# Optimization experiments

Hardware: AMD Instinct MI355X
Metric: run time of the kernel (lower is better)

## Reference

```python
import jax, jax.numpy as jnp
import numpy as np

N, E, G = 50000, 800000, 64          # nodes, edges, graphs in batch
F, HG, HL = 64, 128, 128             # node feat, graph hidden, lin hidden
AVG_LOG = float(np.log(9.0))         # from deg histogram [0]*8+[1]: log(8+1)


def setup_inputs() -> dict:
    key = jax.random.key(0)
    ks = jax.random.split(key, 24)
    def w(k, shape):
        return 0.1 * jax.random.normal(k, shape, jnp.float32)
    return {
        "x": jax.random.normal(ks[0], (N, F), jnp.float32),
        "edge_index": jax.random.randint(ks[1], (2, E), 0, N),
        "edge_attr": jax.random.normal(ks[2], (E, 1), jnp.float32),
        "batch": jnp.sort(jax.random.randint(ks[3], (N,), 0, G)),
        # PNAConv params (towers=1, pre_layers=1, post_layers=1, edge_dim=1)
        "W_edge": w(ks[4], (1, F)),      "b_edge": w(ks[5], (F,)),
        "W_pre": w(ks[6], (3 * F, F)),   "b_pre": w(ks[7], (F,)),
        "W_post": w(ks[8], (13 * F, HG)), "b_post": w(ks[9], (HG,)),
        "W_lin": w(ks[10], (HG, HG)),    "b_lin": w(ks[11], (HG,)),
        # bn1 / fc2 / bn2
        "g1": jnp.ones((HG,)), "be1": jnp.zeros((HG,)),
        "W2": w(ks[12], (HG, HL)), "b2": w(ks[13], (HL,)),
        "g2": jnp.ones((HL,)), "be2": jnp.zeros((HL,)),
        # one resnet block: fc/bn/fc/bn
        "Wr1": w(ks[14], (HL, HL)), "br1": w(ks[15], (HL,)),
        "gr1": jnp.ones((HL,)), "ber1": jnp.zeros((HL,)),
        "Wr2": w(ks[16], (HL, HL)), "br2": w(ks[17], (HL,)),
        "gr2": jnp.ones((HL,)), "ber2": jnp.zeros((HL,)),
        "W_out": w(ks[18], (HL, 1)), "b_out": w(ks[19], (1,)),
    }


def _bn(z, g, b):
    # BatchNorm1d, training mode: biased batch stats, eps=1e-5
    mu = z.mean(0)
    var = ((z - mu) ** 2).mean(0)
    return (z - mu) * jax.lax.rsqrt(var + 1e-5) * g + b


def _pna(x, edge_index, edge_attr, W_edge, b_edge, W_pre, b_pre,
         W_post, b_post, W_lin, b_lin):
    src, dst = edge_index[0], edge_index[1]  # messages flow j->i, aggregate at dst
    e = edge_attr @ W_edge + b_edge                               # [E, F]
    m = jnp.concatenate([x[dst], x[src], e], -1) @ W_pre + b_pre  # [E, F]
    ones_e = jnp.ones((m.shape[0],), m.dtype)
    cnt = jax.ops.segment_sum(ones_e, dst, N)                     # in-degree
    cnt1 = jnp.maximum(cnt, 1.0)
    mean = jax.ops.segment_sum(m, dst, N) / cnt1[:, None]
    mean2 = jax.ops.segment_sum(m * m, dst, N) / cnt1[:, None]
    std = jnp.sqrt(jax.nn.relu(mean2 - mean * mean) + 1e-5)
    has = (cnt > 0)[:, None]
    mn = jnp.where(has, jax.ops.segment_min(m, dst, N), 0.0)
    mx = jnp.where(has, jax.ops.segment_max(m, dst, N), 0.0)
    agg = jnp.concatenate([mean, mn, mx, std], -1)                # [N, 4F]
    amp = (jnp.log(cnt1 + 1.0) / AVG_LOG)[:, None]                # amplification scaler
    out = jnp.concatenate([agg, agg * amp, agg / amp], -1)        # [N, 12F]
    out = jnp.concatenate([x, out], -1) @ W_post + b_post         # [N, HG]
    return out @ W_lin + b_lin                                    # [N, HG]


def reference(x, edge_index, edge_attr, batch,
              W_edge, b_edge, W_pre, b_pre, W_post, b_post, W_lin, b_lin,
              g1, be1, W2, b2, g2, be2,
              Wr1, br1, gr1, ber1, Wr2, br2, gr2, ber2,
              W_out, b_out):
    h = _pna(x, edge_index, edge_attr, W_edge, b_edge, W_pre, b_pre,
             W_post, b_post, W_lin, b_lin)
    # global_mean_pool over graphs
    gc = jnp.maximum(jax.ops.segment_sum(jnp.ones((h.shape[0],), h.dtype), batch, G), 1.0)
    z = jax.ops.segment_sum(h, batch, G) / gc[:, None]            # [G, HG]
    z = jax.nn.relu(_bn(z, g1, be1))
    z = jax.nn.relu(_bn(z @ W2 + b2, g2, be2))
    r = z
    z = jax.nn.relu(_bn(z @ Wr1 + br1, gr1, ber1))
    z = jax.nn.relu(_bn(z @ Wr2 + br2, gr2, ber2) + r)
    return z @ W_out + b_out                                      # [G, 1]
```

## Files before the change

### kernel.cpp

```cpp
#include <hip/hip_runtime.h>
#include <hip/hip_bf16.h>

using bf16 = __hip_bfloat16;

#define F 64
#define HG 128
#define HL 128
#define AVG_LOG_INV 0.45511961331341866f
#define BSH 5
#define BNODES 32
#define BCAP 1024
#define BTILE 8192
#define NBMAX 1664

typedef short short8 __attribute__((ext_vector_type(8)));
typedef float floatx4 __attribute__((ext_vector_type(4)));

__device__ __forceinline__ float b2f(bf16 v) { return __bfloat162float(v); }
__device__ __forceinline__ bf16 f2b(float v) { return __float2bfloat16(v); }
__device__ __forceinline__ short f2bs(float v) { bf16 h = f2b(v); return *(short*)&h; }

__device__ __forceinline__ unsigned packbf2(float x, float y) {
    bf16 a = f2b(x), b = f2b(y);
    unsigned short ua = *(unsigned short*)&a, ub = *(unsigned short*)&b;
    return ((unsigned)ub << 16) | (unsigned)ua;
}

__device__ __forceinline__ float wave_sum(float v) {
    #pragma unroll
    for (int m = 32; m > 0; m >>= 1) v += __shfl_xor(v, m);
    return v;
}

__global__ void k_ab_mfma(const float* __restrict__ x, const float* __restrict__ W_pre,
                          bf16* __restrict__ AB, int N,
                          int* __restrict__ gcur, float* __restrict__ gfeat,
                          int* __restrict__ gcnt, int NB, int GF, int G,
                          const float* __restrict__ W_edge, const float* __restrict__ b_edge,
                          const float* __restrict__ b_pre, float* __restrict__ uc) {
    int gtid = blockIdx.x * blockDim.x + threadIdx.x;
    int gstr = gridDim.x * blockDim.x;
    for (int i = gtid; i < GF; i += gstr) gfeat[i] = 0.f;
    for (int i = gtid; i < NB; i += gstr) gcur[i] = 0;
    for (int i = gtid; i < G; i += gstr) gcnt[i] = 0;
    if (blockIdx.x == 0 && threadIdx.x < 64) {
        int f = threadIdx.x;
        float u = 0.f, c = b_pre[f];
        for (int k = 0; k < 64; k++) {
            float w3 = W_pre[(128 + k) * 64 + f];
            u += W_edge[k] * w3;
            c += b_edge[k] * w3;
        }
        uc[f] = u; uc[64 + f] = c;
    }

    __shared__ unsigned short wt[128 * 72];
    for (int idx = threadIdx.x; idx < 8192; idx += 256) {
        int k = idx >> 7, m = idx & 127;
        float v = W_pre[((m & 64) + k) * 64 + (m & 63)];
        wt[m * 72 + k] = (unsigned short)f2bs(v);
    }
    __syncthreads();

    int lane = threadIdx.x & 63;
    int row = lane & 15, quad = lane >> 4;
    int w = (blockIdx.x * blockDim.x + threadIdx.x) >> 6;
    int nwaves = (gridDim.x * blockDim.x) >> 6;
    int ntiles = (N + 15) >> 4;

    for (int tile = w; tile < ntiles; tile += nwaves) {
        int m0 = tile << 4;
        int node_a = m0 + row; if (node_a >= N) node_a = N - 1;
        short8 a[2];
        #pragma unroll
        for (int h = 0; h < 2; h++) {
            const float* xp = x + (size_t)node_a * 64 + h * 32 + quad * 8;
            floatx4 v0 = *(const floatx4*)xp;
            floatx4 v1 = *(const floatx4*)(xp + 4);
            #pragma unroll
            for (int j = 0; j < 4; j++) { a[h][j] = f2bs(v0[j]); a[h][4 + j] = f2bs(v1[j]); }
        }
        #pragma unroll
        for (int t = 0; t < 8; t++) {
            int fbase = t * 16;
            floatx4 c = {0.f, 0.f, 0.f, 0.f};
            #pragma unroll
            for (int h = 0; h < 2; h++) {
                short8 b = *(const short8*)(wt + (fbase + row) * 72 + h * 32 + quad * 8);
                c = __builtin_amdgcn_mfma_f32_16x16x32_bf16(a[h], b, c, 0, 0, 0);
            }
            #pragma unroll
            for (int r = 0; r < 4; r++) {
                int node = m0 + quad * 4 + r;
                if (node < N) AB[(size_t)node * 128 + fbase + row] = f2b(c[r]);
            }
        }
    }
}

__global__ void k_bucket(const int* __restrict__ ei, const float* __restrict__ ea,
                         int* __restrict__ gcur, int2* __restrict__ gout,
                         int E, int NB) {
    __shared__ int2 recs[BTILE];
    __shared__ int hist[NBMAX], gst[NBMAX], lrk[NBMAX];
    int t = threadIdx.x;
    for (int b = t; b < NB; b += 1024) hist[b] = 0;
    __syncthreads();
    int base = blockIdx.x * BTILE;
    int lim = E - base; if (lim > BTILE) lim = BTILE;
    int nq = lim >> 2;
    const int4* src4 = (const int4*)(ei + base);
    const int4* dst4 = (const int4*)(ei + E + base);
    const float4* ea4 = (const float4*)(ea + base);
    for (int q = t; q < nq; q += 1024) {
        int4 s = src4[q], d = dst4[q];
        float4 v = ea4[q];
        int i = q * 4;
        recs[i]     = make_int2((d.x << 16) | s.x, __float_as_int(v.x));
        recs[i + 1] = make_int2((d.y << 16) | s.y, __float_as_int(v.y));
        recs[i + 2] = make_int2((d.z << 16) | s.z, __float_as_int(v.z));
        recs[i + 3] = make_int2((d.w << 16) | s.w, __float_as_int(v.w));
        atomicAdd(&hist[d.x >> BSH], 1);
        atomicAdd(&hist[d.y >> BSH], 1);
        atomicAdd(&hist[d.z >> BSH], 1);
        atomicAdd(&hist[d.w >> BSH], 1);
    }
    for (int i = (nq << 2) + t; i < lim; i += 1024) {
        int e = base + i;
        int src = ei[e], dst = ei[E + e];
        recs[i] = make_int2((dst << 16) | src, __float_as_int(ea[e]));
        atomicAdd(&hist[dst >> BSH], 1);
    }
    __syncthreads();
    for (int b = t; b < NB; b += 1024) {
        int h = hist[b];
        lrk[b] = 0;
        gst[b] = (h > 0) ? atomicAdd(&gcur[b], h) : 0;
    }
    __syncthreads();
    for (int i = t; i < lim; i += 1024) {
        int2 r = recs[i];
        int b = ((unsigned)r.x) >> (16 + BSH);
        int k = atomicAdd(&lrk[b], 1);
        int pos = gst[b] + k;
        if (pos < BCAP) gout[(size_t)b * BCAP + pos] = r;
    }
}

__global__ void k_edge(const bf16* __restrict__ AB, const int2* __restrict__ gout,
                       const int* __restrict__ gcur, const float* __restrict__ uc,
                       bf16* __restrict__ agg, float* __restrict__ ampv, int N) {
    __shared__ int2 recs[BCAP], sortd[BCAP];
    __shared__ int ncnt[BNODES], nofs[BNODES], nrank[BNODES];
    int t = threadIdx.x;
    int b = blockIdx.x;
    int nn = N - b * BNODES; if (nn > BNODES) nn = BNODES;
    int ecnt = gcur[b]; if (ecnt > BCAP) ecnt = BCAP;

    for (int i = t; i < ecnt; i += 512) recs[i] = gout[(size_t)b * BCAP + i];
    if (t < BNODES) { ncnt[t] = 0; nrank[t] = 0; }
    __syncthreads();
    for (int i = t; i < ecnt; i += 512)
        atomicAdd(&ncnt[((unsigned)recs[i].x >> 16) & (BNODES - 1)], 1);
    __syncthreads();
    if (t < BNODES) {
        int v = ncnt[t], inc = v;
        #pragma unroll
        for (int m = 1; m < BNODES; m <<= 1) { int u = __shfl_up(inc, m); if (t >= m) inc += u; }
        nofs[t] = inc - v;
    }
    __syncthreads();
    for (int i = t; i < ecnt; i += 512) {
        int2 r = recs[i];
        int nl = ((unsigned)r.x >> 16) & (BNODES - 1);
        int k = atomicAdd(&nrank[nl], 1);
        sortd[nofs[nl] + k] = r;
    }
    __syncthreads();

    int lane = t & 63, w = t >> 6;
    int half = lane & 31, hi32 = lane >> 5;
    float2 u2 = *(const float2*)(uc + 2 * half);
    float2 c2 = *(const float2*)(uc + 64 + 2 * half);

    for (int nl = w; nl < nn; nl += 8) {
        int n = b * BNODES + nl;
        int lo = nofs[nl], cnt = ncnt[nl], hi = lo + cnt;

        unsigned apack = *(const unsigned*)(AB + (size_t)n * 128 + 2 * half);
        float acx = __uint_as_float(apack << 16) + c2.x;
        float acy = __uint_as_float(apack & 0xffff0000u) + c2.y;

        float sx = 0.f, sy = 0.f, qx = 0.f, qy = 0.f;
        float mnx = 3.4e38f, mny = 3.4e38f, mxx = -3.4e38f, mxy = -3.4e38f;

        auto acc2 = [&](unsigned bp, float eav) {
            float bx = __uint_as_float(bp << 16);
            float by = __uint_as_float(bp & 0xffff0000u);
            float m0 = fmaf(eav, u2.x, acx) + bx;
            float m1 = fmaf(eav, u2.y, acy) + by;
            sx += m0; qx = fmaf(m0, m0, qx);
            sy += m1; qy = fmaf(m1, m1, qy);
            mnx = fminf(mnx, m0); mxx = fmaxf(mxx, m0);
            mny = fminf(mny, m1); mxy = fmaxf(mxy, m1);
        };
        auto gaddr = [&](int sn) {
            return (const unsigned*)(AB + (size_t)sn * 128 + 64 + 2 * half);
        };

        for (int base = lo; base < hi; base += 64) {
            int nb = hi - base; if (nb > 64) nb = 64;
            int2 rec = (lane < nb) ? sortd[base + lane] : make_int2(0, 0);
            int vsn = rec.x & 0xFFFF;
            float vea = __int_as_float(rec.y);
            int i = 0;
            for (; i + 8 <= nb; i += 8) {
                int sn0 = __shfl(vsn, i + hi32);
                int sn1 = __shfl(vsn, i + 2 + hi32);
                int sn2 = __shfl(vsn, i + 4 + hi32);
                int sn3 = __shfl(vsn, i + 6 + hi32);
                float e0 = __shfl(vea, i + hi32);
                float e1 = __shfl(vea, i + 2 + hi32);
                float e2 = __shfl(vea, i + 4 + hi32);
                float e3 = __shfl(vea, i + 6 + hi32);
                unsigned b0 = *gaddr(sn0);
                unsigned b1 = *gaddr(sn1);
                unsigned b2 = *gaddr(sn2);
                unsigned b3 = *gaddr(sn3);
                acc2(b0, e0); acc2(b1, e1); acc2(b2, e2); acc2(b3, e3);
            }
            for (; i + 2 <= nb; i += 2) {
                int   sn = __shfl(vsn, i + hi32);
                float ev = __shfl(vea, i + hi32);
                acc2(*gaddr(sn), ev);
            }
            if (i < nb) {
                int   sn = __shfl(vsn, i);
                float ev = __shfl(vea, i);
                unsigned bp = *gaddr(sn);
                if (hi32 == 0) acc2(bp, ev);
            }
        }
        sx += __shfl_xor(sx, 32); sy += __shfl_xor(sy, 32);
        qx += __shfl_xor(qx, 32); qy += __shfl_xor(qy, 32);
        mnx = fminf(mnx, __shfl_xor(mnx, 32)); mny = fminf(mny, __shfl_xor(mny, 32));
        mxx = fmaxf(mxx, __shfl_xor(mxx, 32)); mxy = fmaxf(mxy, __shfl_xor(mxy, 32));

        float c1 = (cnt > 0) ? (float)cnt : 1.f;
        float inv = 1.f / c1;
        float mex = sx * inv, mey = sy * inv;
        float vx = qx * inv - mex * mex; if (vx < 0.f) vx = 0.f;
        float vy = qy * inv - mey * mey; if (vy < 0.f) vy = 0.f;
        float sdx = sqrtf(vx + 1e-5f), sdy = sqrtf(vy + 1e-5f);
        if (cnt == 0) { mnx = mny = mxx = mxy = 0.f; }

        size_t ob = (size_t)n * 256 + 2 * half;
        if (hi32 == 0) {
            *(unsigned*)(agg + ob)       = packbf2(mex, mey);
            *(unsigned*)(agg + ob + 64)  = packbf2(mnx, mny);
        } else {
            *(unsigned*)(agg + ob + 128) = packbf2(mxx, mxy);
            *(unsigned*)(agg + ob + 192) = packbf2(sdx, sdy);
        }
        if (lane == 0) ampv[n] = logf(c1 + 1.f) * AVG_LOG_INV;
    }
}

__global__ void k_greduce2(const float* __restrict__ x, const bf16* __restrict__ agg,
                           const float* __restrict__ ampv, const int* __restrict__ batch,
                           float* __restrict__ gfeat, int* __restrict__ gcnt,
                           int N, int chunk) {
    int t = threadIdx.x;
    int lo = blockIdx.x * chunk;
    int hi = lo + chunk; if (hi > N) hi = N;
    if (lo >= hi) return;
    int curg = batch[lo];
    float s1 = 0.f, s2 = 0.f, s3 = 0.f, sx = 0.f;
    int cnt = 0;
    for (int n = lo; n < hi; n++) {
        int g = batch[n];
        if (g != curg) {
            float* gf = gfeat + (size_t)curg * 832;
            unsafeAtomicAdd(&gf[64 + t], s1);
            unsafeAtomicAdd(&gf[320 + t], s2);
            unsafeAtomicAdd(&gf[576 + t], s3);
            if (t < 64) unsafeAtomicAdd(&gf[t], sx);
            if (t == 0) atomicAdd(&gcnt[curg], cnt);
            s1 = s2 = s3 = sx = 0.f; cnt = 0; curg = g;
        }
        float amp = ampv[n];
        float av = b2f(agg[(size_t)n * 256 + t]);
        s1 += av; s2 += av * amp; s3 += av / amp;
        if (t < 64) sx += x[(size_t)n * 64 + t];
        cnt++;
    }
    float* gf = gfeat + (size_t)curg * 832;
    unsafeAtomicAdd(&gf[64 + t], s1);
    unsafeAtomicAdd(&gf[320 + t], s2);
    unsafeAtomicAdd(&gf[576 + t], s3);
    if (t < 64) unsafeAtomicAdd(&gf[t], sx);
    if (t == 0) atomicAdd(&gcnt[curg], cnt);
}

__global__ void k_post1(const float* __restrict__ gfeat, const int* __restrict__ gcnt,
                        const float* __restrict__ W_post, const float* __restrict__ b_post,
                        const float* __restrict__ W_lin, const float* __restrict__ b_lin,
                        float* __restrict__ Zin) {
    int g = blockIdx.x, j = threadIdx.x;
    __shared__ float feat[832];
    __shared__ float z1[128];
    int cg = gcnt[g];
    float r = 1.f / ((cg > 0) ? (float)cg : 1.f);
    for (int i = j; i < 832; i += 128) feat[i] = gfeat[(size_t)g * 832 + i] * r;
    __syncthreads();
    float acc = b_post[j];
    for (int k = 0; k < 832; k++) acc += feat[k] * W_post[k * 128 + j];
    z1[j] = acc;
    __syncthreads();
    float a2 = b_lin[j];
    for (int k = 0; k < 128; k++) a2 += z1[k] * W_lin[k * 128 + j];
    if (cg == 0) a2 = 0.f;
    Zin[g * 128 + j] = a2;
}

__global__ void k_mlpcol(const float* __restrict__ in, const float* __restrict__ W,
                         const float* __restrict__ bias,
                         const float* __restrict__ gamma, const float* __restrict__ beta,
                         const float* __restrict__ res,
                         const float* __restrict__ g_in, const float* __restrict__ be_in,
                         float* __restrict__ outp) {
    __shared__ float A[64 * 129];
    __shared__ float part[4 * 64];
    int t = threadIdx.x;
    int j = blockIdx.x;

    for (int i = t; i < 8192; i += 256) A[(i >> 7) * 129 + (i & 127)] = in[i];
    __syncthreads();

    if (g_in) {
        if (t < 128) {
            int c = t;
            float mu = 0.f;
            for (int r = 0; r < 64; r++) mu += A[r * 129 + c];
            mu *= (1.f / 64.f);
            float var = 0.f;
            for (int r = 0; r < 64; r++) { float d = A[r * 129 + c] - mu; var += d * d; }
            var *= (1.f / 64.f);
            float sc = rsqrtf(var + 1e-5f) * g_in[c], sh = be_in[c];
            for (int r = 0; r < 64; r++) {
                float v = (A[r * 129 + c] - mu) * sc + sh;
                A[r * 129 + c] = v > 0.f ? v : 0.f;
            }
        }
        __syncthreads();
    }

    int r = t & 63, q = t >> 6;
    float acc = 0.f;
    int k0 = q * 32;
    #pragma unroll
    for (int k = 0; k < 32; k++) acc += A[r * 129 + k0 + k] * W[(k0 + k) * 128 + j];
    part[q * 64 + r] = acc;
    __syncthreads();

    if (t < 64) {
        float v = part[t] + part[64 + t] + part[128 + t] + part[192 + t] + bias[j];
        float mu = wave_sum(v) * (1.f / 64.f);
        float d = v - mu;
        float var = wave_sum(d * d) * (1.f / 64.f);
        float o = d * rsqrtf(var + 1e-5f) * gamma[j] + beta[j];
        if (res) o += res[t * 128 + j];
        outp[t * 128 + j] = o > 0.f ? o : 0.f;
    }
}

__global__ void k_out(const float* __restrict__ z4, const float* __restrict__ W_out,
                      const float* b_out, float* __restrict__ out) {
    int g = threadIdx.x;
    float acc = b_out[0];
    for (int j = 0; j < 128; j++) acc += z4[g * 128 + j] * W_out[j];
    out[g] = acc;
}

extern "C" void kernel_launch(void* const* d_in, const int* in_sizes, int n_in,
                              void* d_out, int out_size, void* d_ws, size_t ws_size,
                              hipStream_t stream) {
    const float* x      = (const float*)d_in[0];
    const int*   ei     = (const int*)d_in[1];
    const float* ea     = (const float*)d_in[2];
    const int*   batch  = (const int*)d_in[3];
    const float* W_edge = (const float*)d_in[4];
    const float* b_edge = (const float*)d_in[5];
    const float* W_pre  = (const float*)d_in[6];
    const float* b_pre  = (const float*)d_in[7];
    const float* W_post = (const float*)d_in[8];
    const float* b_post = (const float*)d_in[9];
    const float* W_lin  = (const float*)d_in[10];
    const float* b_lin  = (const float*)d_in[11];
    const float* g1     = (const float*)d_in[12];
    const float* be1    = (const float*)d_in[13];
    const float* W2     = (const float*)d_in[14];
    const float* b2     = (const float*)d_in[15];
    const float* g2     = (const float*)d_in[16];
    const float* be2    = (const float*)d_in[17];
    const float* Wr1    = (const float*)d_in[18];
    const float* br1    = (const float*)d_in[19];
    const float* gr1    = (const float*)d_in[20];
    const float* ber1   = (const float*)d_in[21];
    const float* Wr2    = (const float*)d_in[22];
    const float* br2    = (const float*)d_in[23];
    const float* gr2    = (const float*)d_in[24];
    const float* ber2   = (const float*)d_in[25];
    const float* W_out  = (const float*)d_in[26];
    const float* b_out  = (const float*)d_in[27];
    float* out = (float*)d_out;

    const int N = in_sizes[0] / F;
    const int E = in_sizes[1] / 2;
    const int G = out_size;
    const int NB = (N + BNODES - 1) >> BSH;

    char* p = (char*)d_ws;
    auto alloc = [&](size_t nbytes) { void* r = p; p += (nbytes + 255) & ~(size_t)255; return r; };
    bf16*  AB     = (bf16*)alloc((size_t)N * 128 * sizeof(bf16));
    bf16*  agg    = (bf16*)alloc((size_t)N * 256 * sizeof(bf16));
    float* ampv   = (float*)alloc((size_t)N * sizeof(float));
    int*   gcur   = (int*)alloc((size_t)NB * sizeof(int));
    int2*  gout   = (int2*)alloc((size_t)NB * BCAP * sizeof(int2));
    float* uc     = (float*)alloc(128 * sizeof(float));
    float* gfeat  = (float*)alloc((size_t)G * 832 * sizeof(float));
    int*   gcnt   = (int*)alloc((size_t)G * sizeof(int));
    float* Zin    = (float*)alloc(64 * 128 * sizeof(float));
    float* z2b    = (float*)alloc(64 * 128 * sizeof(float));
    float* z3b    = (float*)alloc(64 * 128 * sizeof(float));
    float* z4b    = (float*)alloc(64 * 128 * sizeof(float));

    const int GF = G * 832;
    const int GRB = 1024;
    const int GRCH = (N + GRB - 1) / GRB;
    const int ABB = ((N + 15) / 16 + 3) / 4;
    const int NBT = (E + BTILE - 1) / BTILE;

    k_ab_mfma<<<ABB, 256, 0, stream>>>(x, W_pre, AB, N, gcur, gfeat, gcnt, NB, GF, G,
                                       W_edge, b_edge, b_pre, uc);
    k_bucket<<<NBT, 1024, 0, stream>>>(ei, ea, gcur, gout, E, NB);
    k_edge<<<NB, 512, 0, stream>>>(AB, gout, gcur, uc, agg, ampv, N);
    k_greduce2<<<GRB, 256, 0, stream>>>(x, agg, ampv, batch, gfeat, gcnt, N, GRCH);
    k_post1<<<G, 128, 0, stream>>>(gfeat, gcnt, W_post, b_post, W_lin, b_lin, Zin);
    k_mlpcol<<<HG, 256, 0, stream>>>(Zin, W2, b2, g2, be2, nullptr, g1, be1, z2b);
    k_mlpcol<<<HL, 256, 0, stream>>>(z2b, Wr1, br1, gr1, ber1, nullptr, nullptr, nullptr, z3b);
    k_mlpcol<<<HL, 256, 0, stream>>>(z3b, Wr2, br2, gr2, ber2, z2b, nullptr, nullptr, z4b);
    k_out<<<1, 64, 0, stream>>>(z4b, W_out, b_out, out);
}
```

Measured before the change: 235.9 us.

## Merge AB GEMM with edge bucketing and fuse MLP tail via grid barrier

Runs the edge bucketing and the node AB MFMA projection in one launch, using disjoint block ranges and a union of shared memory so the two independent stages can overlap. Buffer zeroing moves to a single memset. The five small tail kernels (post projection, three MLP stages, output) become one persistent 128-block kernel that uses atomic grid barriers, removing launch gaps. The barrier depends on all 128 blocks being resident at once, and the bucket tile is halved.

```diff
diff --git a/kernel.cpp b/kernel.cpp
--- a/kernel.cpp
+++ b/kernel.cpp
@@ -10,7 +10,7 @@
 #define BSH 5
 #define BNODES 32
 #define BCAP 1024
-#define BTILE 8192
+#define BTILE2 4096
 #define NBMAX 1664
 
 typedef short short8 __attribute__((ext_vector_type(8)));
@@ -32,19 +32,68 @@
     return v;
 }
 
-__global__ void k_ab_mfma(const float* __restrict__ x, const float* __restrict__ W_pre,
-                          bf16* __restrict__ AB, int N,
-                          int* __restrict__ gcur, float* __restrict__ gfeat,
-                          int* __restrict__ gcnt, int NB, int GF, int G,
-                          const float* __restrict__ W_edge, const float* __restrict__ b_edge,
-                          const float* __restrict__ b_pre, float* __restrict__ uc) {
-    int gtid = blockIdx.x * blockDim.x + threadIdx.x;
-    int gstr = gridDim.x * blockDim.x;
-    for (int i = gtid; i < GF; i += gstr) gfeat[i] = 0.f;
-    for (int i = gtid; i < NB; i += gstr) gcur[i] = 0;
-    for (int i = gtid; i < G; i += gstr) gcnt[i] = 0;
-    if (blockIdx.x == 0 && threadIdx.x < 64) {
-        int f = threadIdx.x;
+union SmAB {
+    struct { int2 recs[BTILE2]; int hist[NBMAX]; int gst[NBMAX]; int lrk[NBMAX]; } bk;
+    unsigned short wt[128 * 72];
+};
+
+__global__ void k_abbucket(const float* __restrict__ x, const float* __restrict__ W_pre,
+                           bf16* __restrict__ AB, int N,
+                           const int* __restrict__ ei, const float* __restrict__ ea,
+                           int* __restrict__ gcur, int2* __restrict__ gout, int E, int NB,
+                           const float* __restrict__ W_edge, const float* __restrict__ b_edge,
+                           const float* __restrict__ b_pre, float* __restrict__ uc, int NBT) {
+    __shared__ SmAB sm;
+    int t = threadIdx.x;
+    int bid = blockIdx.x;
+
+    if (bid < NBT) {
+        for (int b = t; b < NB; b += 512) sm.bk.hist[b] = 0;
+        __syncthreads();
+        int base = bid * BTILE2;
+        int lim = E - base; if (lim > BTILE2) lim = BTILE2;
+        int nq = ((E & 3) == 0) ? (lim >> 2) : 0;
+        const int4* src4 = (const int4*)(ei + base);
+        const int4* dst4 = (const int4*)(ei + E + base);
+        const float4* ea4 = (const float4*)(ea + base);
+        for (int q = t; q < nq; q += 512) {
+            int4 s = src4[q], d = dst4[q];
+            float4 v = ea4[q];
+            int i = q * 4;
+            sm.bk.recs[i]     = make_int2((d.x << 16) | s.x, __float_as_int(v.x));
+            sm.bk.recs[i + 1] = make_int2((d.y << 16) | s.y, __float_as_int(v.y));
+            sm.bk.recs[i + 2] = make_int2((d.z << 16) | s.z, __float_as_int(v.z));
+            sm.bk.recs[i + 3] = make_int2((d.w << 16) | s.w, __float_as_int(v.w));
+            atomicAdd(&sm.bk.hist[d.x >> BSH], 1);
+            atomicAdd(&sm.bk.hist[d.y >> BSH], 1);
+            atomicAdd(&sm.bk.hist[d.z >> BSH], 1);
+            atomicAdd(&sm.bk.hist[d.w >> BSH], 1);
+        }
+        for (int i = (nq << 2) + t; i < lim; i += 512) {
+            int e = base + i;
+            int src = ei[e], dst = ei[E + e];
+            sm.bk.recs[i] = make_int2((dst << 16) | src, __float_as_int(ea[e]));
+            atomicAdd(&sm.bk.hist[dst >> BSH], 1);
+        }
+        __syncthreads();
+        for (int b = t; b < NB; b += 512) {
+            int h = sm.bk.hist[b];
+            sm.bk.lrk[b] = 0;
+            sm.bk.gst[b] = (h > 0) ? atomicAdd(&gcur[b], h) : 0;
+        }
+        __syncthreads();
+        for (int i = t; i < lim; i += 512) {
+            int2 r = sm.bk.recs[i];
+            int b = ((unsigned)r.x) >> (16 + BSH);
+            int k = atomicAdd(&sm.bk.lrk[b], 1);
+            int pos = sm.bk.gst[b] + k;
+            if (pos < BCAP) gout[(size_t)b * BCAP + pos] = r;
+        }
+        return;
+    }
+
+    if (bid == gridDim.x - 1 && t < 64) {
+        int f = t;
         float u = 0.f, c = b_pre[f];
         for (int k = 0; k < 64; k++) {
             float w3 = W_pre[(128 + k) * 64 + f];
@@ -53,19 +102,17 @@
         }
         uc[f] = u; uc[64 + f] = c;
     }
-
-    __shared__ unsigned short wt[128 * 72];
-    for (int idx = threadIdx.x; idx < 8192; idx += 256) {
+    for (int idx = t; idx < 8192; idx += 512) {
         int k = idx >> 7, m = idx & 127;
-        float v = W_pre[((m & 64) + k) * 64 + (m & 63)];
-        wt[m * 72 + k] = (unsigned short)f2bs(v);
-    }
-    __syncthreads();
-
-    int lane = threadIdx.x & 63;
+        sm.wt[m * 72 + k] = (unsigned short)f2bs(W_pre[((m & 64) + k) * 64 + (m & 63)]);
+    }
+    __syncthreads();
+
+    int lane = t & 63;
     int row = lane & 15, quad = lane >> 4;
-    int w = (blockIdx.x * blockDim.x + threadIdx.x) >> 6;
-    int nwaves = (gridDim.x * blockDim.x) >> 6;
+    int abid = bid - NBT;
+    int w = abid * 8 + (t >> 6);
+    int nwaves = (gridDim.x - NBT) * 8;
     int ntiles = (N + 15) >> 4;
 
     for (int tile = w; tile < ntiles; tile += nwaves) {
@@ -81,12 +128,12 @@
             for (int j = 0; j < 4; j++) { a[h][j] = f2bs(v0[j]); a[h][4 + j] = f2bs(v1[j]); }
         }
         #pragma unroll
-        for (int t = 0; t < 8; t++) {
-            int fbase = t * 16;
+        for (int s = 0; s < 8; s++) {
+            int fbase = s * 16;
             floatx4 c = {0.f, 0.f, 0.f, 0.f};
             #pragma unroll
             for (int h = 0; h < 2; h++) {
-                short8 b = *(const short8*)(wt + (fbase + row) * 72 + h * 32 + quad * 8);
+                short8 b = *(const short8*)(sm.wt + (fbase + row) * 72 + h * 32 + quad * 8);
                 c = __builtin_amdgcn_mfma_f32_16x16x32_bf16(a[h], b, c, 0, 0, 0);
             }
             #pragma unroll
@@ -95,55 +142,6 @@
                 if (node < N) AB[(size_t)node * 128 + fbase + row] = f2b(c[r]);
             }
         }
-    }
-}
-
-__global__ void k_bucket(const int* __restrict__ ei, const float* __restrict__ ea,
-                         int* __restrict__ gcur, int2* __restrict__ gout,
-                         int E, int NB) {
-    __shared__ int2 recs[BTILE];
-    __shared__ int hist[NBMAX], gst[NBMAX], lrk[NBMAX];
-    int t = threadIdx.x;
-    for (int b = t; b < NB; b += 1024) hist[b] = 0;
-    __syncthreads();
-    int base = blockIdx.x * BTILE;
-    int lim = E - base; if (lim > BTILE) lim = BTILE;
-    int nq = lim >> 2;
-    const int4* src4 = (const int4*)(ei + base);
-    const int4* dst4 = (const int4*)(ei + E + base);
-    const float4* ea4 = (const float4*)(ea + base);
-    for (int q = t; q < nq; q += 1024) {
-        int4 s = src4[q], d = dst4[q];
-        float4 v = ea4[q];
-        int i = q * 4;
-        recs[i]     = make_int2((d.x << 16) | s.x, __float_as_int(v.x));
-        recs[i + 1] = make_int2((d.y << 16) | s.y, __float_as_int(v.y));
-        recs[i + 2] = make_int2((d.z << 16) | s.z, __float_as_int(v.z));
-        recs[i + 3] = make_int2((d.w << 16) | s.w, __float_as_int(v.w));
-        atomicAdd(&hist[d.x >> BSH], 1);
-        atomicAdd(&hist[d.y >> BSH], 1);
-        atomicAdd(&hist[d.z >> BSH], 1);
-        atomicAdd(&hist[d.w >> BSH], 1);
-    }
-    for (int i = (nq << 2) + t; i < lim; i += 1024) {
-        int e = base + i;
-        int src = ei[e], dst = ei[E + e];
-        recs[i] = make_int2((dst << 16) | src, __float_as_int(ea[e]));
-        atomicAdd(&hist[dst >> BSH], 1);
-    }
-    __syncthreads();
-    for (int b = t; b < NB; b += 1024) {
-        int h = hist[b];
-        lrk[b] = 0;
-        gst[b] = (h > 0) ? atomicAdd(&gcur[b], h) : 0;
-    }
-    __syncthreads();
-    for (int i = t; i < lim; i += 1024) {
-        int2 r = recs[i];
-        int b = ((unsigned)r.x) >> (16 + BSH);
-        int k = atomicAdd(&lrk[b], 1);
-        int pos = gst[b] + k;
-        if (pos < BCAP) gout[(size_t)b * BCAP + pos] = r;
     }
 }
 
@@ -302,41 +300,25 @@
     if (t == 0) atomicAdd(&gcnt[curg], cnt);
 }
 
-__global__ void k_post1(const float* __restrict__ gfeat, const int* __restrict__ gcnt,
-                        const float* __restrict__ W_post, const float* __restrict__ b_post,
-                        const float* __restrict__ W_lin, const float* __restrict__ b_lin,
-                        float* __restrict__ Zin) {
-    int g = blockIdx.x, j = threadIdx.x;
-    __shared__ float feat[832];
-    __shared__ float z1[128];
-    int cg = gcnt[g];
-    float r = 1.f / ((cg > 0) ? (float)cg : 1.f);
-    for (int i = j; i < 832; i += 128) feat[i] = gfeat[(size_t)g * 832 + i] * r;
-    __syncthreads();
-    float acc = b_post[j];
-    for (int k = 0; k < 832; k++) acc += feat[k] * W_post[k * 128 + j];
-    z1[j] = acc;
-    __syncthreads();
-    float a2 = b_lin[j];
-    for (int k = 0; k < 128; k++) a2 += z1[k] * W_lin[k * 128 + j];
-    if (cg == 0) a2 = 0.f;
-    Zin[g * 128 + j] = a2;
-}
-
-__global__ void k_mlpcol(const float* __restrict__ in, const float* __restrict__ W,
-                         const float* __restrict__ bias,
-                         const float* __restrict__ gamma, const float* __restrict__ beta,
-                         const float* __restrict__ res,
-                         const float* __restrict__ g_in, const float* __restrict__ be_in,
-                         float* __restrict__ outp) {
-    __shared__ float A[64 * 129];
-    __shared__ float part[4 * 64];
+__device__ __forceinline__ void gridbar(int* bar, int target) {
+    __syncthreads();
+    if (threadIdx.x == 0) {
+        __threadfence();
+        atomicAdd(bar, 1);
+        while (__hip_atomic_load(bar, __ATOMIC_ACQUIRE, __HIP_MEMORY_SCOPE_AGENT) < target) {}
+    }
+    __syncthreads();
+}
+
+__device__ void mlp_stage(const float* __restrict__ in, const float* __restrict__ W,
+                          const float* __restrict__ bias,
+                          const float* __restrict__ gamma, const float* __restrict__ beta,
+                          const float* __restrict__ res,
+                          const float* __restrict__ g_in, const float* __restrict__ be_in,
+                          float* __restrict__ outp, float* A, float* part, int j) {
     int t = threadIdx.x;
-    int j = blockIdx.x;
-
     for (int i = t; i < 8192; i += 256) A[(i >> 7) * 129 + (i & 127)] = in[i];
     __syncthreads();
-
     if (g_in) {
         if (t < 128) {
             int c = t;
@@ -354,7 +336,6 @@
         }
         __syncthreads();
     }
-
     int r = t & 63, q = t >> 6;
     float acc = 0.f;
     int k0 = q * 32;
@@ -362,7 +343,6 @@
     for (int k = 0; k < 32; k++) acc += A[r * 129 + k0 + k] * W[(k0 + k) * 128 + j];
     part[q * 64 + r] = acc;
     __syncthreads();
-
     if (t < 64) {
         float v = part[t] + part[64 + t] + part[128 + t] + part[192 + t] + bias[j];
         float mu = wave_sum(v) * (1.f / 64.f);
@@ -372,14 +352,57 @@
         if (res) o += res[t * 128 + j];
         outp[t * 128 + j] = o > 0.f ? o : 0.f;
     }
-}
-
-__global__ void k_out(const float* __restrict__ z4, const float* __restrict__ W_out,
-                      const float* b_out, float* __restrict__ out) {
-    int g = threadIdx.x;
-    float acc = b_out[0];
-    for (int j = 0; j < 128; j++) acc += z4[g * 128 + j] * W_out[j];
-    out[g] = acc;
+    __syncthreads();
+}
+
+__global__ void __launch_bounds__(256) k_tail(
+        const float* __restrict__ gfeat, const int* __restrict__ gcnt,
+        const float* __restrict__ W_post, const float* __restrict__ b_post,
+        const float* __restrict__ W_lin, const float* __restrict__ b_lin,
+        float* __restrict__ Zin,
+        const float* g1, const float* be1,
+        const float* __restrict__ W2, const float* b2, const float* g2, const float* be2,
+        const float* __restrict__ Wr1, const float* br1, const float* gr1, const float* ber1,
+        const float* __restrict__ Wr2, const float* br2, const float* gr2, const float* ber2,
+        const float* __restrict__ W_out, const float* b_out,
+        float* __restrict__ z2b, float* __restrict__ z3b, float* __restrict__ z4b,
+        float* __restrict__ out, int* bar, int G) {
+    __shared__ float A[64 * 129];
+    __shared__ float part[256];
+    __shared__ float feat[832];
+    __shared__ float z1[128];
+    int t = threadIdx.x, bid = blockIdx.x;
+
+    if (bid < G) {
+        int cg = gcnt[bid];
+        float r = 1.f / ((cg > 0) ? (float)cg : 1.f);
+        for (int i = t; i < 832; i += 256) feat[i] = gfeat[(size_t)bid * 832 + i] * r;
+        __syncthreads();
+        if (t < 128) {
+            float acc = b_post[t];
+            for (int k = 0; k < 832; k++) acc += feat[k] * W_post[k * 128 + t];
+            z1[t] = acc;
+        }
+        __syncthreads();
+        if (t < 128) {
+            float a2 = b_lin[t];
+            for (int k = 0; k < 128; k++) a2 += z1[k] * W_lin[k * 128 + t];
+            if (cg == 0) a2 = 0.f;
+            Zin[bid * 128 + t] = a2;
+        }
+    }
+    gridbar(bar, 128);
+    mlp_stage(Zin, W2, b2, g2, be2, nullptr, g1, be1, z2b, A, part, bid);
+    gridbar(bar, 256);
+    mlp_stage(z2b, Wr1, br1, gr1, ber1, nullptr, nullptr, nullptr, z3b, A, part, bid);
+    gridbar(bar, 384);
+    mlp_stage(z3b, Wr2, br2, gr2, ber2, z2b, nullptr, nullptr, z4b, A, part, bid);
+    gridbar(bar, 512);
+    if (bid == 0 && t < 64) {
+        float acc = b_out[0];
+        for (int j = 0; j < 128; j++) acc += z4b[t * 128 + j] * W_out[j];
+        out[t] = acc;
+    }
 }
 
 extern "C" void kernel_launch(void* const* d_in, const int* in_sizes, int n_in,
@@ -419,36 +442,37 @@
     const int E = in_sizes[1] / 2;
     const int G = out_size;
     const int NB = (N + BNODES - 1) >> BSH;
+    const int GF = G * 832;
 
     char* p = (char*)d_ws;
     auto alloc = [&](size_t nbytes) { void* r = p; p += (nbytes + 255) & ~(size_t)255; return r; };
     bf16*  AB     = (bf16*)alloc((size_t)N * 128 * sizeof(bf16));
     bf16*  agg    = (bf16*)alloc((size_t)N * 256 * sizeof(bf16));
     float* ampv   = (float*)alloc((size_t)N * sizeof(float));
-    int*   gcur   = (int*)alloc((size_t)NB * sizeof(int));
     int2*  gout   = (int2*)alloc((size_t)NB * BCAP * sizeof(int2));
     float* uc     = (float*)alloc(128 * sizeof(float));
-    float* gfeat  = (float*)alloc((size_t)G * 832 * sizeof(float));
-    int*   gcnt   = (int*)alloc((size_t)G * sizeof(int));
     float* Zin    = (float*)alloc(64 * 128 * sizeof(float));
     float* z2b    = (float*)alloc(64 * 128 * sizeof(float));
     float* z3b    = (float*)alloc(64 * 128 * sizeof(float));
     float* z4b    = (float*)alloc(64 * 128 * sizeof(float));
-
-    const int GF = G * 832;
+    size_t zbytes = (size_t)(1 + NB + G) * sizeof(int) + (size_t)GF * sizeof(float);
+    int*   bar    = (int*)alloc(zbytes);
+    int*   gcur   = bar + 1;
+    int*   gcnt   = gcur + NB;
+    float* gfeat  = (float*)(gcnt + G);
+
     const int GRB = 1024;
     const int GRCH = (N + GRB - 1) / GRB;
-    const int ABB = ((N + 15) / 16 + 3) / 4;
-    const int NBT = (E + BTILE - 1) / BTILE;
-
-    k_ab_mfma<<<ABB, 256, 0, stream>>>(x, W_pre, AB, N, gcur, gfeat, gcnt, NB, GF, G,
-                                       W_edge, b_edge, b_pre, uc);
-    k_bucket<<<NBT, 1024, 0, stream>>>(ei, ea, gcur, gout, E, NB);
+    const int NBT = (E + BTILE2 - 1) / BTILE2;
+    const int ABB = (((N + 15) / 16) + 7) / 8;
+
+    hipMemsetAsync(bar, 0, zbytes, stream);
+    k_abbucket<<<NBT + ABB, 512, 0, stream>>>(x, W_pre, AB, N, ei, ea, gcur, gout, E, NB,
+                                              W_edge, b_edge, b_pre, uc, NBT);
     k_edge<<<NB, 512, 0, stream>>>(AB, gout, gcur, uc, agg, ampv, N);
     k_greduce2<<<GRB, 256, 0, stream>>>(x, agg, ampv, batch, gfeat, gcnt, N, GRCH);
-    k_post1<<<G, 128, 0, stream>>>(gfeat, gcnt, W_post, b_post, W_lin, b_lin, Zin);
-    k_mlpcol<<<HG, 256, 0, stream>>>(Zin, W2, b2, g2, be2, nullptr, g1, be1, z2b);
-    k_mlpcol<<<HL, 256, 0, stream>>>(z2b, Wr1, br1, gr1, ber1, nullptr, nullptr, nullptr, z3b);
-    k_mlpcol<<<HL, 256, 0, stream>>>(z3b, Wr2, br2, gr2, ber2, z2b, nullptr, nullptr, z4b);
-    k_out<<<1, 64, 0, stream>>>(z4b, W_out, b_out, out);
-}
+    k_tail<<<128, 256, 0, stream>>>(gfeat, gcnt, W_post, b_post, W_lin, b_lin, Zin,
+                                    g1, be1, W2, b2, g2, be2,
+                                    Wr1, br1, gr1, ber1, Wr2, br2, gr2, ber2,
+                                    W_out, b_out, z2b, z3b, z4b, out, bar, G);
+}
```

Result: slower. 274.8 us (+16.5%).
